# Kernel tuning notes

Measured on AMD Instinct MI355X. Metric: run time of the kernel, lower is better.

## Reference

```python
import jax, jax.numpy as jnp
import numpy as np

EPS = 1e-8
KERNEL_K = 25
SCALES = (1, 2, 3)


def setup_inputs() -> dict:
    key = jax.random.key(0)
    k1, k2, k3 = jax.random.split(key, 3)
    B, D = 4096, 256
    features = jax.random.normal(k1, (B, D), dtype=jnp.float32)
    scores = jax.random.normal(k2, (B, 1), dtype=jnp.float32)
    labels = jax.random.randint(k3, (B,), 0, 6, dtype=jnp.int64)
    return {"features": features, "scores": scores, "labels": labels}


def _affinity(features):
    # squared pairwise euclidean distances (cdist(...,p=2)**2)
    sq = jnp.sum(features * features, axis=1)
    dist_sq = jnp.maximum(sq[:, None] + sq[None, :] - 2.0 * (features @ features.T), 0.0)
    B = features.shape[0]
    k = min(KERNEL_K, B)
    neg_topk, topk_idx = jax.lax.top_k(-dist_sq, k)  # smallest-k per row
    topk_dist = -neg_topk
    sigma = jnp.mean(jnp.sqrt(topk_dist + EPS), axis=1, keepdims=True)  # [B,1]
    sigma_mat = sigma @ sigma.T
    knn_mask = jnp.zeros((B, B), dtype=bool).at[jnp.arange(B)[:, None], topk_idx].set(True)
    mutual = knn_mask & knn_mask.T
    W = jnp.exp(-dist_sq / (sigma_mat + EPS))
    return W * mutual.astype(W.dtype)


def reference(features, scores, labels):
    B = features.shape[0]
    W_feat = _affinity(features)
    lab = labels.reshape(-1, 1).astype(features.dtype)
    direction_mask = (lab <= lab.T).astype(features.dtype)
    W = W_feat * direction_mask + jnp.eye(B, dtype=features.dtype)
    P = W / (jnp.sum(W, axis=1, keepdims=True) + EPS)
    penalty = jax.nn.relu(scores - scores.T)  # [B,B]
    loss = jnp.asarray(0.0, dtype=features.dtype)
    P_t = P
    max_scale = max(SCALES)
    for t in range(1, max_scale + 1):
        if t in SCALES:
            loss = loss + (1.0 / t) * jnp.mean(jnp.sum(P_t * penalty, axis=1))
        if t < max_scale:
            P_t = P_t @ P
    return loss
```

## Files before the change

kernel.cpp:

```cpp
#include <hip/hip_runtime.h>
#include <math.h>
#include <float.h>

#define NB 4096
#define ND 256
#define NK 25
#define EPSF 1e-8f
#define CAP 256

typedef __attribute__((ext_vector_type(8))) short bf16x8;
typedef __attribute__((ext_vector_type(4))) float f32x4;

#define GLD_LDS16(gp, lp)                                                   \
    __builtin_amdgcn_global_load_lds(                                       \
        (const __attribute__((address_space(1))) void*)(uintptr_t)(gp),     \
        (__attribute__((address_space(3))) void*)(uint32_t)(uintptr_t)(lp), \
        16, 0, 0)

__device__ inline short f2bf(float x) {
    unsigned u = __float_as_uint(x);
    return (short)((u + 0x7FFF + ((u >> 16) & 1)) >> 16);
}

__global__ __launch_bounds__(64) void prep_kernel(const float* __restrict__ f,
                                                  short* __restrict__ fh,
                                                  float* __restrict__ sq) {
    int row  = blockIdx.x;
    int lane = threadIdx.x;
    float4 v = ((const float4*)(f + (size_t)row * ND))[lane];
    float acc = v.x * v.x + v.y * v.y + v.z * v.z + v.w * v.w;
    *(short4*)(fh + (size_t)row * ND + lane * 4) =
        make_short4(f2bf(v.x), f2bf(v.y), f2bf(v.z), f2bf(v.w));
#pragma unroll
    for (int off = 32; off; off >>= 1) acc += __shfl_down(acc, off);
    if (lane == 0) sq[row] = acc;
}

#define BM 128
#define BK 64
__global__ __launch_bounds__(256) void gram_kernel(const short* __restrict__ fh,
                                                   const float* __restrict__ sq,
                                                   float* __restrict__ dist) {
    __shared__ __align__(16) short As[BM * BK];
    __shared__ __align__(16) short Bs[BM * BK];
    int b   = blockIdx.x;
    int ti  = (b >> 5) * BM;
    int tj  = (b & 31) * BM;
    int tid = threadIdx.x;
    int w = tid >> 6, lane = tid & 63;
    int wr = w >> 1, wc = w & 1;
    int fr = lane & 15, fq = lane >> 4;

    f32x4 acc[4][4];
#pragma unroll
    for (int m = 0; m < 4; ++m)
#pragma unroll
        for (int n = 0; n < 4; ++n) acc[m][n] = (f32x4){0.f, 0.f, 0.f, 0.f};

    int srow = lane >> 3;
    int scol = (lane & 7) * 8;

    for (int s = 0; s < 4; ++s) {
        int k0 = s * 64;
#pragma unroll
        for (int i = 0; i < 4; ++i) {
            int c   = 4 * w + i;
            int row = c * 8 + srow;
            GLD_LDS16(fh + (size_t)(ti + row) * ND + k0 + scol, As + c * 512);
            GLD_LDS16(fh + (size_t)(tj + row) * ND + k0 + scol, Bs + c * 512);
        }
        __syncthreads();
#pragma unroll
        for (int kk = 0; kk < 2; ++kk) {
            bf16x8 af[4], bfr[4];
#pragma unroll
            for (int m = 0; m < 4; ++m)
                af[m] = *(const bf16x8*)(As + (wr * 64 + m * 16 + fr) * 64 + kk * 32 + fq * 8);
#pragma unroll
            for (int n = 0; n < 4; ++n)
                bfr[n] = *(const bf16x8*)(Bs + (wc * 64 + n * 16 + fr) * 64 + kk * 32 + fq * 8);
#pragma unroll
            for (int m = 0; m < 4; ++m)
#pragma unroll
                for (int n = 0; n < 4; ++n)
                    acc[m][n] = __builtin_amdgcn_mfma_f32_16x16x32_bf16(af[m], bfr[n], acc[m][n], 0, 0, 0);
        }
        __syncthreads();
    }

#pragma unroll
    for (int m = 0; m < 4; ++m) {
#pragma unroll
        for (int j = 0; j < 4; ++j) {
            int gi = ti + wr * 64 + m * 16 + fq * 4 + j;
            float si = sq[gi];
            float* drow = dist + (size_t)gi * NB + tj + wc * 64;
#pragma unroll
            for (int n = 0; n < 4; ++n) {
                float d = si + sq[tj + wc * 64 + n * 16 + fr] - 2.f * acc[m][n][j];
                drow[n * 16 + fr] = fmaxf(d, 0.f);
            }
        }
    }
}

__global__ __launch_bounds__(256) void topk4_kernel(const float* __restrict__ dist,
                                                    int* __restrict__ idxk,
                                                    float* __restrict__ dk,
                                                    float* __restrict__ sigma) {
    int wid  = threadIdx.x >> 6;
    int lane = threadIdx.x & 63;
    int row  = blockIdx.x * 4 + wid;
    __shared__ float cval[4][CAP];
    __shared__ int   cidx[4][CAP];

    float v[64];
    const float4* src = (const float4*)(dist + (size_t)row * NB);
#pragma unroll
    for (int c = 0; c < 16; ++c) {
        float4 q = src[c * 64 + lane];
        v[c * 4 + 0] = q.x; v[c * 4 + 1] = q.y;
        v[c * 4 + 2] = q.z; v[c * 4 + 3] = q.w;
    }

    float mx = v[0], sm = v[0];
#pragma unroll
    for (int e = 1; e < 64; ++e) { mx = fmaxf(mx, v[e]); sm += v[e]; }
#pragma unroll
    for (int off = 32; off; off >>= 1) {
        mx = fmaxf(mx, __shfl_xor(mx, off));
        sm += __shfl_xor(sm, off);
    }
    float mu = sm * (1.0f / NB);

    int c0 = 0;
#pragma unroll
    for (int e = 0; e < 64; ++e) c0 += (v[e] < mu) ? 1 : 0;
#pragma unroll
    for (int off = 32; off; off >>= 1) c0 += __shfl_xor(c0, off);
    float lo = 0.f, hi = mu;
    int cnt_hi = c0;
    if (cnt_hi < NK) { hi = mx * 1.000001f + 1e-20f; cnt_hi = NB; }

    for (int it = 0; it < 40; ++it) {
        if (cnt_hi <= 64) break;
        float mid = 0.5f * (lo + hi);
        if (mid <= lo || mid >= hi) break;
        int c = 0;
#pragma unroll
        for (int e = 0; e < 64; ++e) c += (v[e] < mid) ? 1 : 0;
#pragma unroll
        for (int off = 32; off; off >>= 1) c += __shfl_xor(c, off);
        if (c >= NK) { hi = mid; cnt_hi = c; } else { lo = mid; }
    }

    float Thi = hi;
    unsigned long long ltmask = (1ull << lane) - 1ull;
    int cnt = 0;
#pragma unroll
    for (int e = 0; e < 64; ++e) {
        bool p = (v[e] < Thi);
        unsigned long long m = __ballot(p);
        if (p) {
            int pos = cnt + __popcll(m & ltmask);
            if (pos < CAP) {
                cval[wid][pos] = v[e];
                cidx[wid][pos] = ((e >> 2) * 64 + lane) * 4 + (e & 3);
            }
        }
        cnt += __popcll(m);
    }
    cnt = min(cnt, CAP);

    if (cnt <= 64) {
        float x  = (lane < cnt) ? cval[wid][lane] : FLT_MAX;
        int   xi = (lane < cnt) ? cidx[wid][lane] : 0x7fffffff;
        int rank = 0;
        for (int s = 1; s < 64; ++s) {
            int   sl = (lane + s) & 63;
            float y  = __shfl(x, sl);
            int   yi = __shfl(xi, sl);
            rank += (y < x || (y == x && yi < xi)) ? 1 : 0;
        }
        bool sel = (lane < cnt) && (rank < NK);
        if (sel) {
            idxk[row * NK + rank] = xi;
            dk[row * NK + rank]   = x;
        }
        float t = sel ? sqrtf(x + EPSF) : 0.f;
#pragma unroll
        for (int off = 32; off; off >>= 1) t += __shfl_xor(t, off);
        if (lane == 0) sigma[row] = t * (1.0f / NK);
    } else {
        float ssum = 0.f;
        for (int it = 0; it < NK; ++it) {
            float bv = FLT_MAX; int bi = NB; int bp = -1;
            for (int r = lane; r < cnt; r += 64) {
                float cv = cval[wid][r]; int ci = cidx[wid][r];
                if (cv < bv || (cv == bv && ci < bi)) { bv = cv; bi = ci; bp = r; }
            }
#pragma unroll
            for (int off = 32; off; off >>= 1) {
                float ov = __shfl_xor(bv, off);
                int   oi = __shfl_xor(bi, off);
                int   op = __shfl_xor(bp, off);
                if (ov < bv || (ov == bv && oi < bi)) { bv = ov; bi = oi; bp = op; }
            }
            if (lane == 0) {
                idxk[row * NK + it] = bi;
                dk[row * NK + it]   = bv;
                cval[wid][bp] = FLT_MAX;
            }
            bv = __shfl(bv, 0);
            ssum += sqrtf(bv + EPSF);
        }
        if (lane == 0) sigma[row] = ssum * (1.0f / NK);
    }
}

__global__ __launch_bounds__(64) void buildp_kernel(const int* __restrict__ idxk,
                                                    const float* __restrict__ dk,
                                                    const float* __restrict__ sigma,
                                                    const int* __restrict__ labels,
                                                    const float* __restrict__ scores,
                                                    float* __restrict__ pval,
                                                    float* __restrict__ bs,
                                                    float2* __restrict__ cs) {
    int row  = blockIdx.x;
    int lane = threadIdx.x;
    __shared__ float sb[32];
    __shared__ float sp[32];

    float w = 0.f;
    int j = 0;
    if (lane < NK) {
        j = idxk[row * NK + lane];
        bool mut = false;
        for (int n = 0; n < NK; ++n) mut |= (idxk[j * NK + n] == row);
        bool dir = labels[row] <= labels[j];
        float sij = sigma[row] * sigma[j] + EPSF;
        w = (mut && dir) ? expf(-dk[row * NK + lane] / sij) : 0.f;
        if (j == row) w += 1.f;
    }
    float rs = w;
#pragma unroll
    for (int off = 32; off; off >>= 1) rs += __shfl_down(rs, off);
    rs = __shfl(rs, 0);
    float pv = (lane < NK) ? w / (rs + EPSF) : 0.f;
    if (lane < NK) pval[row * NK + lane] = pv;

    float sj = (lane < NK) ? scores[j] : FLT_MAX;
    int rank = 0;
#pragma unroll
    for (int u = 0; u < NK; ++u) {
        float su = __shfl(sj, u);
        rank += (su < sj || (su == sj && u < lane)) ? 1 : 0;
    }
    if (lane < 32) { sb[lane] = FLT_MAX; sp[lane] = 0.f; }
    __syncthreads();
    if (lane < NK) { sb[rank] = sj; sp[rank] = pv; }
    __syncthreads();

    float b = sb[lane & 31];
    float p = sp[lane & 31];
    float c  = p;
    float s2 = p * b;
#pragma unroll
    for (int off = 1; off < 32; off <<= 1) {
        float oc = __shfl_up(c, off);
        float os = __shfl_up(s2, off);
        if (lane >= off) { c += oc; s2 += os; }
    }
    float ce = __shfl_up(c, 1);
    float se = __shfl_up(s2, 1);
    if (lane == 0) { ce = 0.f; se = 0.f; }
    if (lane < 32) {
        bs[row * 32 + lane] = b;
        cs[row * 32 + lane] = make_float2(ce, se);
    }
}

__global__ __launch_bounds__(256) void hval_kernel(const int* __restrict__ idxk,
                                                   const float* __restrict__ pval,
                                                   const float* __restrict__ scores,
                                                   const float* __restrict__ bs,
                                                   const float2* __restrict__ cs,
                                                   float* __restrict__ Gval,
                                                   float* __restrict__ Hval) {
    int wid  = threadIdx.x >> 6;
    int lane = threadIdx.x & 63;
    int j    = blockIdx.x * 4 + wid;
    __shared__ float2 slab[4][NK][26];

    int  ln = (lane < NK) ? lane : NK - 1;
    int  q  = idxk[j * NK + ln];
    float p = (lane < NK) ? pval[j * NK + lane] : 0.f;
    float sqv = scores[q];

    float4 bq[7];
    const float4* b4 = (const float4*)(bs + q * 32);
#pragma unroll
    for (int t = 0; t < 7; ++t) bq[t] = b4[t];
    const float4* c4 = (const float4*)(cs + q * 32);
    if (lane < NK) {
#pragma unroll
        for (int t = 0; t < 13; ++t)
            *(float4*)&slab[wid][lane][t * 2] = c4[t];
    }

    float bjj = bs[j * 32 + lane];
    int posj = 0;
#pragma unroll
    for (int r = 0; r < NK; ++r)
        posj += (__shfl(bjj, r) < sqv) ? 1 : 0;
    float2 cj = cs[j * 32 + posj];
    if (lane < NK) Gval[j * 32 + lane] = sqv * cj.x - cj.y;

    __syncthreads();

    for (int u = 0; u < NK; ++u) {
        float x = __shfl(sqv, u);
        int pos = 0;
#pragma unroll
        for (int t = 0; t < 7; ++t) {
            float4 b = bq[t];
            pos += (b.x < x) + (b.y < x) + (b.z < x) + (b.w < x);
        }
        float2 ch = slab[wid][ln][pos];
        float g = p * (x * ch.x - ch.y);
#pragma unroll
        for (int off = 32; off; off >>= 1) g += __shfl_xor(g, off);
        if (lane == 0) Hval[j * 32 + u] = g;
    }
}

__global__ __launch_bounds__(256) void loss_kernel(const float* __restrict__ scores,
                                                   const int* __restrict__ idxk,
                                                   const float* __restrict__ pval,
                                                   const float* __restrict__ Gval,
                                                   const float* __restrict__ Hval,
                                                   float* __restrict__ partial) {
    int wid  = threadIdx.x >> 6;
    int lane = threadIdx.x & 63;
    int i    = blockIdx.x * 4 + wid;
    float si = scores[i];
    float acc = 0.f;
    if (lane < NK) {
        int   jm = idxk[i * NK + lane];
        float pm = pval[i * NK + lane];
        float sj = scores[jm];
        int slot = -1;
        const int* row = idxk + jm * NK;
#pragma unroll
        for (int n = 0; n < NK; ++n)
            if (row[n] == i) slot = n;
        float g = 0.f, h = 0.f;
        if (slot >= 0) {
            g = Gval[jm * 32 + slot];
            h = Hval[jm * 32 + slot];
        }
        acc = pm * (fmaxf(si - sj, 0.f) + 0.5f * g + (1.f / 3.f) * h);
    }
#pragma unroll
    for (int off = 32; off; off >>= 1) acc += __shfl_xor(acc, off);
    if (lane == 0) partial[i] = acc;
}

__global__ __launch_bounds__(256) void reduce_kernel(const float* __restrict__ partial,
                                                     float* __restrict__ out) {
    int tid = threadIdx.x;
    __shared__ float red[4];
    float a = 0.f;
    for (int t = tid; t < NB / 4; t += 256) {
        float4 p = ((const float4*)partial)[t];
        a += p.x + p.y + p.z + p.w;
    }
#pragma unroll
    for (int off = 32; off; off >>= 1) a += __shfl_xor(a, off);
    if ((tid & 63) == 0) red[tid >> 6] = a;
    __syncthreads();
    if (tid == 0) out[0] = (red[0] + red[1] + red[2] + red[3]) * (1.0f / NB);
}

extern "C" void kernel_launch(void* const* d_in, const int* in_sizes, int n_in,
                              void* d_out, int out_size, void* d_ws, size_t ws_size,
                              hipStream_t stream) {
    const float* features = (const float*)d_in[0];
    const float* scores   = (const float*)d_in[1];
    const int*   labels   = (const int*)d_in[2];
    float* out = (float*)d_out;

    char* ws = (char*)d_ws;
    size_t off = 0;
    float*  dist    = (float*) (ws + off); off += (size_t)NB * NB * 4;
    short*  fh      = (short*) (ws + off); off += (size_t)NB * ND * 2;
    float*  sq      = (float*) (ws + off); off += (size_t)NB * 4;
    int*    idxk    = (int*)   (ws + off); off += (size_t)NB * NK * 4;
    float*  dk      = (float*) (ws + off); off += (size_t)NB * NK * 4;
    float*  sigma   = (float*) (ws + off); off += (size_t)NB * 4;
    float*  pval    = (float*) (ws + off); off += (size_t)NB * NK * 4;
    float*  bs      = (float*) (ws + off); off += (size_t)NB * 32 * 4;
    float2* cs      = (float2*)(ws + off); off += (size_t)NB * 32 * 8;
    float*  Gval    = (float*) (ws + off); off += (size_t)NB * 32 * 4;
    float*  Hval    = (float*) (ws + off); off += (size_t)NB * 32 * 4;
    float*  partial = (float*) (ws + off); off += (size_t)NB * 4;

    prep_kernel<<<NB, 64, 0, stream>>>(features, fh, sq);
    gram_kernel<<<(NB / BM) * (NB / BM), 256, 0, stream>>>(fh, sq, dist);
    topk4_kernel<<<NB / 4, 256, 0, stream>>>(dist, idxk, dk, sigma);
    buildp_kernel<<<NB, 64, 0, stream>>>(idxk, dk, sigma, labels, scores, pval, bs, cs);
    hval_kernel<<<NB / 4, 256, 0, stream>>>(idxk, pval, scores, bs, cs, Gval, Hval);
    loss_kernel<<<NB / 4, 256, 0, stream>>>(scores, idxk, pval, Gval, Hval, partial);
    reduce_kernel<<<1, 256, 0, stream>>>(partial, out);
}
```

Baseline: 101.4 us.

## Filter kNN candidates in gram epilogue instead of materializing full distance matrix

The gram kernel no longer writes the full 4096x4096 distance matrix. It keeps only entries below a per-row threshold, estimated from the statistics of the squared norms, and appends them to a per-row candidate list with atomics. A small top-k kernel ranks these candidates. Rows whose candidate count falls outside the valid range go to a fallback kernel that recomputes the row in full. This removes a 64MB write and re-read, but adds global atomics, an extra launch of 4096 mostly-idle blocks, and a slow path whose cost depends on how well the threshold fits the data.

```diff
diff --git a/kernel.cpp b/kernel.cpp
--- a/kernel.cpp
+++ b/kernel.cpp
@@ -7,6 +7,8 @@
 #define NK 25
 #define EPSF 1e-8f
 #define CAP 256
+#define CAP_FB 1024
+#define CTGT 192
 
 typedef __attribute__((ext_vector_type(8))) short bf16x8;
 typedef __attribute__((ext_vector_type(4))) float f32x4;
@@ -20,6 +22,9 @@
 __device__ inline short f2bf(float x) {
     unsigned u = __float_as_uint(x);
     return (short)((u + 0x7FFF + ((u >> 16) & 1)) >> 16);
+}
+__device__ inline float bf2f(short s) {
+    return __uint_as_float(((unsigned)(unsigned short)s) << 16);
 }
 
 __global__ __launch_bounds__(64) void prep_kernel(const float* __restrict__ f,
@@ -36,13 +41,40 @@
     if (lane == 0) sq[row] = acc;
 }
 
+__global__ __launch_bounds__(256) void mstat_kernel(const float* __restrict__ sq,
+                                                    float* __restrict__ T,
+                                                    int* __restrict__ cnt,
+                                                    int* __restrict__ flag) {
+    int tid = threadIdx.x;
+    __shared__ float r1[4], r2[4];
+    float a1 = 0.f, a2 = 0.f;
+    for (int t = tid; t < NB; t += 256) { float s = sq[t]; a1 += s; a2 += s * s; }
+#pragma unroll
+    for (int off = 32; off; off >>= 1) { a1 += __shfl_xor(a1, off); a2 += __shfl_xor(a2, off); }
+    if ((tid & 63) == 0) { r1[tid >> 6] = a1; r2[tid >> 6] = a2; }
+    __syncthreads();
+    float M1 = (r1[0] + r1[1] + r1[2] + r1[3]) * (1.0f / NB);
+    float M2 = (r2[0] + r2[1] + r2[2] + r2[3]) * (1.0f / NB);
+    float varsq = fmaxf(M2 - M1 * M1, 0.f);
+    for (int t = tid; t < NB; t += 256) {
+        float s = sq[t];
+        float sig = sqrtf(varsq + 4.f * s);
+        T[t] = s + M1 - 2.0f * sig;
+        cnt[t]  = 0;
+        flag[t] = 0;
+    }
+}
+
 #define BM 128
 #define BK 64
 __global__ __launch_bounds__(256) void gram_kernel(const short* __restrict__ fh,
                                                    const float* __restrict__ sq,
-                                                   float* __restrict__ dist) {
+                                                   const float* __restrict__ T,
+                                                   int* __restrict__ cnt,
+                                                   float2* __restrict__ cand) {
     __shared__ __align__(16) short As[BM * BK];
     __shared__ __align__(16) short Bs[BM * BK];
+    __shared__ float sT[BM];
     int b   = blockIdx.x;
     int ti  = (b >> 5) * BM;
     int tj  = (b & 31) * BM;
@@ -51,6 +83,8 @@
     int wr = w >> 1, wc = w & 1;
     int fr = lane & 15, fq = lane >> 4;
 
+    if (tid < BM) sT[tid] = T[ti + tid];
+
     f32x4 acc[4][4];
 #pragma unroll
     for (int m = 0; m < 4; ++m)
@@ -92,129 +126,170 @@
     for (int m = 0; m < 4; ++m) {
 #pragma unroll
         for (int j = 0; j < 4; ++j) {
-            int gi = ti + wr * 64 + m * 16 + fq * 4 + j;
+            int rl = wr * 64 + m * 16 + fq * 4 + j;
+            int gi = ti + rl;
             float si = sq[gi];
-            float* drow = dist + (size_t)gi * NB + tj + wc * 64;
+            float Tr = sT[rl];
 #pragma unroll
             for (int n = 0; n < 4; ++n) {
-                float d = si + sq[tj + wc * 64 + n * 16 + fr] - 2.f * acc[m][n][j];
-                drow[n * 16 + fr] = fmaxf(d, 0.f);
+                int col = tj + wc * 64 + n * 16 + fr;
+                float d = fmaxf(si + sq[col] - 2.f * acc[m][n][j], 0.f);
+                if (d < Tr) {
+                    int pos = atomicAdd(&cnt[gi], 1);
+                    if (pos < CAP)
+                        cand[(size_t)gi * CAP + pos] = make_float2(d, __int_as_float(col));
+                }
             }
         }
     }
 }
 
-__global__ __launch_bounds__(256) void topk4_kernel(const float* __restrict__ dist,
+__global__ __launch_bounds__(256) void topk5_kernel(const float2* __restrict__ cand,
+                                                    const int* __restrict__ cnt,
+                                                    int* __restrict__ flag,
                                                     int* __restrict__ idxk,
                                                     float* __restrict__ dk,
                                                     float* __restrict__ sigma) {
     int wid  = threadIdx.x >> 6;
     int lane = threadIdx.x & 63;
     int row  = blockIdx.x * 4 + wid;
-    __shared__ float cval[4][CAP];
-    __shared__ int   cidx[4][CAP];
-
-    float v[64];
-    const float4* src = (const float4*)(dist + (size_t)row * NB);
-#pragma unroll
-    for (int c = 0; c < 16; ++c) {
-        float4 q = src[c * 64 + lane];
-        v[c * 4 + 0] = q.x; v[c * 4 + 1] = q.y;
-        v[c * 4 + 2] = q.z; v[c * 4 + 3] = q.w;
-    }
-
-    float mx = v[0], sm = v[0];
-#pragma unroll
-    for (int e = 1; e < 64; ++e) { mx = fmaxf(mx, v[e]); sm += v[e]; }
-#pragma unroll
-    for (int off = 32; off; off >>= 1) {
-        mx = fmaxf(mx, __shfl_xor(mx, off));
-        sm += __shfl_xor(sm, off);
-    }
-    float mu = sm * (1.0f / NB);
-
-    int c0 = 0;
-#pragma unroll
-    for (int e = 0; e < 64; ++e) c0 += (v[e] < mu) ? 1 : 0;
-#pragma unroll
-    for (int off = 32; off; off >>= 1) c0 += __shfl_xor(c0, off);
-    float lo = 0.f, hi = mu;
-    int cnt_hi = c0;
-    if (cnt_hi < NK) { hi = mx * 1.000001f + 1e-20f; cnt_hi = NB; }
-
-    for (int it = 0; it < 40; ++it) {
-        if (cnt_hi <= 64) break;
-        float mid = 0.5f * (lo + hi);
-        if (mid <= lo || mid >= hi) break;
+    int c = cnt[row];
+    if (c < NK || c > CAP) { if (lane == 0) flag[row] = 1; return; }
+    int slots = (c + 63) >> 6;
+
+    float v[4]; int id[4];
+#pragma unroll
+    for (int k = 0; k < 4; ++k) {
+        int p = lane + 64 * k;
+        if (p < c) {
+            float2 q = cand[(size_t)row * CAP + p];
+            v[k] = q.x; id[k] = __float_as_int(q.y);
+        } else { v[k] = FLT_MAX; id[k] = 0x7fffffff; }
+    }
+    int rank[4] = {0, 0, 0, 0};
+    for (int s = 0; s < 64; ++s) {
+        int sl = (lane + s) & 63;
+#pragma unroll
+        for (int k2 = 0; k2 < 4; ++k2) {
+            if (k2 < slots) {
+                float y  = __shfl(v[k2], sl);
+                int   yi = __shfl(id[k2], sl);
+#pragma unroll
+                for (int k = 0; k < 4; ++k) {
+                    if (k < slots) {
+                        bool lt = (y < v[k]) || (y == v[k] && yi < id[k]);
+                        rank[k] += lt ? 1 : 0;
+                    }
+                }
+            }
+        }
+    }
+    float t = 0.f;
+#pragma unroll
+    for (int k = 0; k < 4; ++k) {
+        if (k < slots && v[k] != FLT_MAX && rank[k] < NK) {
+            idxk[row * NK + rank[k]] = id[k];
+            dk[row * NK + rank[k]]   = v[k];
+            t += sqrtf(v[k] + EPSF);
+        }
+    }
+#pragma unroll
+    for (int off = 32; off; off >>= 1) t += __shfl_xor(t, off);
+    if (lane == 0) sigma[row] = t * (1.0f / NK);
+}
+
+__global__ __launch_bounds__(256) void fixup_kernel(const short* __restrict__ fh,
+                                                    const float* __restrict__ sq,
+                                                    const int* __restrict__ flag,
+                                                    int* __restrict__ idxk,
+                                                    float* __restrict__ dk,
+                                                    float* __restrict__ sigma) {
+    int row = blockIdx.x;
+    if (flag[row] == 0) return;
+    __shared__ float rowv[NB];
+    __shared__ float frv[ND];
+    __shared__ float cval[CAP_FB];
+    __shared__ int   cidx[CAP_FB];
+    __shared__ int   red[4];
+    __shared__ float redf[4];
+    __shared__ int   s_cnt;
+    int tid = threadIdx.x;
+
+    for (int a = tid; a < ND; a += 256) frv[a] = bf2f(fh[(size_t)row * ND + a]);
+    __syncthreads();
+    float sqr = sq[row];
+    for (int c = tid; c < NB; c += 256) {
+        const short4* fc4 = (const short4*)(fh + (size_t)c * ND);
+        float acc = 0.f;
+        for (int a4 = 0; a4 < ND / 4; ++a4) {
+            short4 q = fc4[a4];
+            acc += frv[a4 * 4 + 0] * bf2f(q.x) + frv[a4 * 4 + 1] * bf2f(q.y)
+                 + frv[a4 * 4 + 2] * bf2f(q.z) + frv[a4 * 4 + 3] * bf2f(q.w);
+        }
+        rowv[c] = fmaxf(sqr + sq[c] - 2.f * acc, 0.f);
+    }
+    __syncthreads();
+
+    float mx = 0.f;
+    for (int t = tid; t < NB; t += 256) mx = fmaxf(mx, rowv[t]);
+#pragma unroll
+    for (int off = 32; off; off >>= 1) mx = fmaxf(mx, __shfl_xor(mx, off));
+    if ((tid & 63) == 0) redf[tid >> 6] = mx;
+    __syncthreads();
+    mx = fmaxf(fmaxf(redf[0], redf[1]), fmaxf(redf[2], redf[3]));
+
+    unsigned lo = 0u, hi = __float_as_uint(mx) + 1u;
+    int cnt_hi = NB;
+    for (int it = 0; it < 34; ++it) {
+        if (cnt_hi <= CTGT || hi <= lo + 1u) break;
+        unsigned mid = (lo + hi) >> 1;
+        float Tm = __uint_as_float(mid);
         int c = 0;
-#pragma unroll
-        for (int e = 0; e < 64; ++e) c += (v[e] < mid) ? 1 : 0;
+        for (int t = tid; t < NB; t += 256) c += (rowv[t] < Tm) ? 1 : 0;
 #pragma unroll
         for (int off = 32; off; off >>= 1) c += __shfl_xor(c, off);
+        __syncthreads();
+        if ((tid & 63) == 0) red[tid >> 6] = c;
+        __syncthreads();
+        c = red[0] + red[1] + red[2] + red[3];
         if (c >= NK) { hi = mid; cnt_hi = c; } else { lo = mid; }
     }
-
-    float Thi = hi;
-    unsigned long long ltmask = (1ull << lane) - 1ull;
-    int cnt = 0;
-#pragma unroll
-    for (int e = 0; e < 64; ++e) {
-        bool p = (v[e] < Thi);
-        unsigned long long m = __ballot(p);
-        if (p) {
-            int pos = cnt + __popcll(m & ltmask);
-            if (pos < CAP) {
-                cval[wid][pos] = v[e];
-                cidx[wid][pos] = ((e >> 2) * 64 + lane) * 4 + (e & 3);
-            }
-        }
-        cnt += __popcll(m);
-    }
-    cnt = min(cnt, CAP);
-
-    if (cnt <= 64) {
-        float x  = (lane < cnt) ? cval[wid][lane] : FLT_MAX;
-        int   xi = (lane < cnt) ? cidx[wid][lane] : 0x7fffffff;
-        int rank = 0;
-        for (int s = 1; s < 64; ++s) {
-            int   sl = (lane + s) & 63;
-            float y  = __shfl(x, sl);
-            int   yi = __shfl(xi, sl);
-            rank += (y < x || (y == x && yi < xi)) ? 1 : 0;
-        }
-        bool sel = (lane < cnt) && (rank < NK);
-        if (sel) {
-            idxk[row * NK + rank] = xi;
-            dk[row * NK + rank]   = x;
-        }
-        float t = sel ? sqrtf(x + EPSF) : 0.f;
-#pragma unroll
-        for (int off = 32; off; off >>= 1) t += __shfl_xor(t, off);
-        if (lane == 0) sigma[row] = t * (1.0f / NK);
-    } else {
+    float Thi = __uint_as_float(hi);
+    if (tid == 0) s_cnt = 0;
+    __syncthreads();
+    for (int t = tid; t < NB; t += 256) {
+        if (rowv[t] < Thi) {
+            int p = atomicAdd(&s_cnt, 1);
+            if (p < CAP_FB) { cval[p] = rowv[t]; cidx[p] = t; }
+        }
+    }
+    __syncthreads();
+    int cnt = min(s_cnt, CAP_FB);
+
+    if (tid < 64) {
         float ssum = 0.f;
         for (int it = 0; it < NK; ++it) {
             float bv = FLT_MAX; int bi = NB; int bp = -1;
-            for (int r = lane; r < cnt; r += 64) {
-                float cv = cval[wid][r]; int ci = cidx[wid][r];
+            for (int r = tid; r < cnt; r += 64) {
+                float cv = cval[r]; int ci = cidx[r];
                 if (cv < bv || (cv == bv && ci < bi)) { bv = cv; bi = ci; bp = r; }
             }
 #pragma unroll
             for (int off = 32; off; off >>= 1) {
-                float ov = __shfl_xor(bv, off);
-                int   oi = __shfl_xor(bi, off);
-                int   op = __shfl_xor(bp, off);
+                float ov = __shfl_down(bv, off);
+                int   oi = __shfl_down(bi, off);
+                int   op = __shfl_down(bp, off);
                 if (ov < bv || (ov == bv && oi < bi)) { bv = ov; bi = oi; bp = op; }
             }
-            if (lane == 0) {
+            bp = __shfl(bp, 0); bv = __shfl(bv, 0); bi = __shfl(bi, 0);
+            if (tid == 0) {
                 idxk[row * NK + it] = bi;
                 dk[row * NK + it]   = bv;
-                cval[wid][bp] = FLT_MAX;
+                cval[bp] = FLT_MAX;
             }
-            bv = __shfl(bv, 0);
             ssum += sqrtf(bv + EPSF);
         }
-        if (lane == 0) sigma[row] = ssum * (1.0f / NK);
+        if (tid == 0) sigma[row] = ssum * (1.0f / NK);
     }
 }
 
@@ -392,9 +467,12 @@
 
     char* ws = (char*)d_ws;
     size_t off = 0;
-    float*  dist    = (float*) (ws + off); off += (size_t)NB * NB * 4;
+    float2* cand    = (float2*)(ws + off); off += (size_t)NB * CAP * 8;
     short*  fh      = (short*) (ws + off); off += (size_t)NB * ND * 2;
     float*  sq      = (float*) (ws + off); off += (size_t)NB * 4;
+    float*  T       = (float*) (ws + off); off += (size_t)NB * 4;
+    int*    cnt     = (int*)   (ws + off); off += (size_t)NB * 4;
+    int*    flag    = (int*)   (ws + off); off += (size_t)NB * 4;
     int*    idxk    = (int*)   (ws + off); off += (size_t)NB * NK * 4;
     float*  dk      = (float*) (ws + off); off += (size_t)NB * NK * 4;
     float*  sigma   = (float*) (ws + off); off += (size_t)NB * 4;
@@ -406,8 +484,10 @@
     float*  partial = (float*) (ws + off); off += (size_t)NB * 4;
 
     prep_kernel<<<NB, 64, 0, stream>>>(features, fh, sq);
-    gram_kernel<<<(NB / BM) * (NB / BM), 256, 0, stream>>>(fh, sq, dist);
-    topk4_kernel<<<NB / 4, 256, 0, stream>>>(dist, idxk, dk, sigma);
+    mstat_kernel<<<1, 256, 0, stream>>>(sq, T, cnt, flag);
+    gram_kernel<<<(NB / BM) * (NB / BM), 256, 0, stream>>>(fh, sq, T, cnt, cand);
+    topk5_kernel<<<NB / 4, 256, 0, stream>>>(cand, cnt, flag, idxk, dk, sigma);
+    fixup_kernel<<<NB, 256, 0, stream>>>(fh, sq, flag, idxk, dk, sigma);
     buildp_kernel<<<NB, 64, 0, stream>>>(idxk, dk, sigma, labels, scores, pval, bs, cs);
     hval_kernel<<<NB / 4, 256, 0, stream>>>(idxk, pval, scores, bs, cs, Gval, Hval);
     loss_kernel<<<NB / 4, 256, 0, stream>>>(scores, idxk, pval, Gval, Hval, partial);
```

Measured after the change: 173.4 us. 70.9% more time.

## Predict per-row top-k threshold from norm statistics and use block-per-row selection

Applied to the files above, without the earlier changes.

Adds a small kernel that estimates, for each row, a distance threshold from the mean and variance of squared norms. The top-k kernel then filters candidates against that threshold in a single pass, falling back to bisection only when the candidate count falls outside [NK, CAP]. The kernel moves from one wavefront per row to one 256-thread block per row, which gathers candidates with shared-memory atomics and ranks them by counting. This removes the usual bisection passes over the row but depends on the threshold holding for Gaussian-like inputs; the fallback keeps the result exact.

```diff
diff --git a/kernel.cpp b/kernel.cpp
--- a/kernel.cpp
+++ b/kernel.cpp
@@ -34,6 +34,25 @@
 #pragma unroll
     for (int off = 32; off; off >>= 1) acc += __shfl_down(acc, off);
     if (lane == 0) sq[row] = acc;
+}
+
+__global__ __launch_bounds__(256) void mstat_kernel(const float* __restrict__ sq,
+                                                    float* __restrict__ T) {
+    int tid = threadIdx.x;
+    __shared__ float r1[4], r2[4];
+    float a1 = 0.f, a2 = 0.f;
+    for (int t = tid; t < NB; t += 256) { float s = sq[t]; a1 += s; a2 += s * s; }
+#pragma unroll
+    for (int off = 32; off; off >>= 1) { a1 += __shfl_xor(a1, off); a2 += __shfl_xor(a2, off); }
+    if ((tid & 63) == 0) { r1[tid >> 6] = a1; r2[tid >> 6] = a2; }
+    __syncthreads();
+    float M1 = (r1[0] + r1[1] + r1[2] + r1[3]) * (1.0f / NB);
+    float M2 = (r2[0] + r2[1] + r2[2] + r2[3]) * (1.0f / NB);
+    float varsq = fmaxf(M2 - M1 * M1, 0.f);
+    for (int t = tid; t < NB; t += 256) {
+        float s = sq[t];
+        T[t] = s + M1 - 2.0f * sqrtf(varsq + 4.f * s);
+    }
 }
 
 #define BM 128
@@ -104,117 +123,116 @@
     }
 }
 
-__global__ __launch_bounds__(256) void topk4_kernel(const float* __restrict__ dist,
+__global__ __launch_bounds__(256) void topk8_kernel(const float* __restrict__ dist,
+                                                    const float* __restrict__ T,
                                                     int* __restrict__ idxk,
                                                     float* __restrict__ dk,
                                                     float* __restrict__ sigma) {
-    int wid  = threadIdx.x >> 6;
-    int lane = threadIdx.x & 63;
-    int row  = blockIdx.x * 4 + wid;
-    __shared__ float cval[4][CAP];
-    __shared__ int   cidx[4][CAP];
-
-    float v[64];
+    int row = blockIdx.x;
+    int tid = threadIdx.x;
+    __shared__ float cval[CAP];
+    __shared__ int   cidx[CAP];
+    __shared__ float ssq[NK];
+    __shared__ int   s_cnt;
+    __shared__ int   red[4];
+
+    if (tid == 0) s_cnt = 0;
+    __syncthreads();
+
+    float Tr = T[row];
     const float4* src = (const float4*)(dist + (size_t)row * NB);
-#pragma unroll
-    for (int c = 0; c < 16; ++c) {
-        float4 q = src[c * 64 + lane];
-        v[c * 4 + 0] = q.x; v[c * 4 + 1] = q.y;
-        v[c * 4 + 2] = q.z; v[c * 4 + 3] = q.w;
-    }
-
-    float mx = v[0], sm = v[0];
-#pragma unroll
-    for (int e = 1; e < 64; ++e) { mx = fmaxf(mx, v[e]); sm += v[e]; }
-#pragma unroll
-    for (int off = 32; off; off >>= 1) {
-        mx = fmaxf(mx, __shfl_xor(mx, off));
-        sm += __shfl_xor(sm, off);
-    }
-    float mu = sm * (1.0f / NB);
-
-    int c0 = 0;
-#pragma unroll
-    for (int e = 0; e < 64; ++e) c0 += (v[e] < mu) ? 1 : 0;
-#pragma unroll
-    for (int off = 32; off; off >>= 1) c0 += __shfl_xor(c0, off);
-    float lo = 0.f, hi = mu;
-    int cnt_hi = c0;
-    if (cnt_hi < NK) { hi = mx * 1.000001f + 1e-20f; cnt_hi = NB; }
-
-    for (int it = 0; it < 40; ++it) {
-        if (cnt_hi <= 64) break;
-        float mid = 0.5f * (lo + hi);
-        if (mid <= lo || mid >= hi) break;
-        int c = 0;
-#pragma unroll
-        for (int e = 0; e < 64; ++e) c += (v[e] < mid) ? 1 : 0;
-#pragma unroll
-        for (int off = 32; off; off >>= 1) c += __shfl_xor(c, off);
-        if (c >= NK) { hi = mid; cnt_hi = c; } else { lo = mid; }
-    }
-
-    float Thi = hi;
-    unsigned long long ltmask = (1ull << lane) - 1ull;
-    int cnt = 0;
-#pragma unroll
-    for (int e = 0; e < 64; ++e) {
-        bool p = (v[e] < Thi);
-        unsigned long long m = __ballot(p);
-        if (p) {
-            int pos = cnt + __popcll(m & ltmask);
+
+    float4 q0 = src[0 * 256 + tid];
+    float4 q1 = src[1 * 256 + tid];
+    float4 q2 = src[2 * 256 + tid];
+    float4 q3 = src[3 * 256 + tid];
+    float xs[16] = {q0.x, q0.y, q0.z, q0.w, q1.x, q1.y, q1.z, q1.w,
+                    q2.x, q2.y, q2.z, q2.w, q3.x, q3.y, q3.z, q3.w};
+#pragma unroll
+    for (int e = 0; e < 16; ++e) {
+        if (xs[e] < Tr) {
+            int pos = atomicAdd(&s_cnt, 1);
             if (pos < CAP) {
-                cval[wid][pos] = v[e];
-                cidx[wid][pos] = ((e >> 2) * 64 + lane) * 4 + (e & 3);
+                cval[pos] = xs[e];
+                cidx[pos] = ((e >> 2) * 256 + tid) * 4 + (e & 3);
             }
         }
-        cnt += __popcll(m);
-    }
-    cnt = min(cnt, CAP);
-
-    if (cnt <= 64) {
-        float x  = (lane < cnt) ? cval[wid][lane] : FLT_MAX;
-        int   xi = (lane < cnt) ? cidx[wid][lane] : 0x7fffffff;
-        int rank = 0;
-        for (int s = 1; s < 64; ++s) {
-            int   sl = (lane + s) & 63;
-            float y  = __shfl(x, sl);
-            int   yi = __shfl(xi, sl);
-            rank += (y < x || (y == x && yi < xi)) ? 1 : 0;
-        }
-        bool sel = (lane < cnt) && (rank < NK);
-        if (sel) {
-            idxk[row * NK + rank] = xi;
-            dk[row * NK + rank]   = x;
-        }
-        float t = sel ? sqrtf(x + EPSF) : 0.f;
-#pragma unroll
-        for (int off = 32; off; off >>= 1) t += __shfl_xor(t, off);
-        if (lane == 0) sigma[row] = t * (1.0f / NK);
-    } else {
-        float ssum = 0.f;
-        for (int it = 0; it < NK; ++it) {
-            float bv = FLT_MAX; int bi = NB; int bp = -1;
-            for (int r = lane; r < cnt; r += 64) {
-                float cv = cval[wid][r]; int ci = cidx[wid][r];
-                if (cv < bv || (cv == bv && ci < bi)) { bv = cv; bi = ci; bp = r; }
+    }
+    __syncthreads();
+    int cnt = s_cnt;
+
+    if (cnt < NK || cnt > CAP) {
+        float s1 = 0.f, mx = 0.f;
+#pragma unroll
+        for (int e = 0; e < 16; ++e) { s1 += xs[e]; mx = fmaxf(mx, xs[e]); }
+#pragma unroll
+        for (int off = 32; off; off >>= 1) { s1 += __shfl_xor(s1, off); mx = fmaxf(mx, __shfl_xor(mx, off)); }
+        __syncthreads();
+        if ((tid & 63) == 0) { ((float*)red)[tid >> 6] = s1; }
+        __syncthreads();
+        s1 = ((float*)red)[0] + ((float*)red)[1] + ((float*)red)[2] + ((float*)red)[3];
+        __syncthreads();
+        if ((tid & 63) == 0) { ((float*)red)[tid >> 6] = mx; }
+        __syncthreads();
+        mx = fmaxf(fmaxf(((float*)red)[0], ((float*)red)[1]),
+                   fmaxf(((float*)red)[2], ((float*)red)[3]));
+        float mu = s1 * (1.0f / NB);
+        float lo = 0.f, hi = mx * 1.000001f + 1e-20f;
+        int cnt_hi = NB;
+        for (int it = 0; it < 40; ++it) {
+            if (cnt_hi >= NK && cnt_hi <= CAP) break;
+            float mid = (cnt_hi > CAP) ? 0.5f * (lo + hi) : mu;
+            mid = 0.5f * (lo + hi);
+            if (mid <= lo || mid >= hi) break;
+            int c = 0;
+#pragma unroll
+            for (int e = 0; e < 16; ++e) c += (xs[e] < mid) ? 1 : 0;
+#pragma unroll
+            for (int off = 32; off; off >>= 1) c += __shfl_xor(c, off);
+            __syncthreads();
+            if ((tid & 63) == 0) red[tid >> 6] = c;
+            __syncthreads();
+            c = red[0] + red[1] + red[2] + red[3];
+            if (c >= NK) { hi = mid; cnt_hi = c; } else { lo = mid; }
+            __syncthreads();
+        }
+        Tr = hi;
+        if (tid == 0) s_cnt = 0;
+        __syncthreads();
+#pragma unroll
+        for (int e = 0; e < 16; ++e) {
+            if (xs[e] < Tr) {
+                int pos = atomicAdd(&s_cnt, 1);
+                if (pos < CAP) {
+                    cval[pos] = xs[e];
+                    cidx[pos] = ((e >> 2) * 256 + tid) * 4 + (e & 3);
+                }
             }
-#pragma unroll
-            for (int off = 32; off; off >>= 1) {
-                float ov = __shfl_xor(bv, off);
-                int   oi = __shfl_xor(bi, off);
-                int   op = __shfl_xor(bp, off);
-                if (ov < bv || (ov == bv && oi < bi)) { bv = ov; bi = oi; bp = op; }
-            }
-            if (lane == 0) {
-                idxk[row * NK + it] = bi;
-                dk[row * NK + it]   = bv;
-                cval[wid][bp] = FLT_MAX;
-            }
-            bv = __shfl(bv, 0);
-            ssum += sqrtf(bv + EPSF);
-        }
-        if (lane == 0) sigma[row] = ssum * (1.0f / NK);
+        }
+        __syncthreads();
+        cnt = min(s_cnt, CAP);
+    }
+
+    float x  = (tid < cnt) ? cval[tid] : FLT_MAX;
+    int   xi = (tid < cnt) ? cidx[tid] : 0x7fffffff;
+    int rank = 0;
+    for (int r = 0; r < cnt; ++r) {
+        float y  = cval[r];
+        int   yi = cidx[r];
+        rank += (y < x || (y == x && yi < xi)) ? 1 : 0;
+    }
+    bool sel = (tid < cnt) && (rank < NK);
+    if (sel) {
+        idxk[row * NK + rank] = xi;
+        dk[row * NK + rank]   = x;
+        ssq[rank] = sqrtf(x + EPSF);
+    }
+    __syncthreads();
+    if (tid == 0) {
+        float t = 0.f;
+#pragma unroll
+        for (int r = 0; r < NK; ++r) t += ssq[r];
+        sigma[row] = t * (1.0f / NK);
     }
 }
 
@@ -395,6 +413,7 @@
     float*  dist    = (float*) (ws + off); off += (size_t)NB * NB * 4;
     short*  fh      = (short*) (ws + off); off += (size_t)NB * ND * 2;
     float*  sq      = (float*) (ws + off); off += (size_t)NB * 4;
+    float*  T       = (float*) (ws + off); off += (size_t)NB * 4;
     int*    idxk    = (int*)   (ws + off); off += (size_t)NB * NK * 4;
     float*  dk      = (float*) (ws + off); off += (size_t)NB * NK * 4;
     float*  sigma   = (float*) (ws + off); off += (size_t)NB * 4;
@@ -406,8 +425,9 @@
     float*  partial = (float*) (ws + off); off += (size_t)NB * 4;
 
     prep_kernel<<<NB, 64, 0, stream>>>(features, fh, sq);
+    mstat_kernel<<<1, 256, 0, stream>>>(sq, T);
     gram_kernel<<<(NB / BM) * (NB / BM), 256, 0, stream>>>(fh, sq, dist);
-    topk4_kernel<<<NB / 4, 256, 0, stream>>>(dist, idxk, dk, sigma);
+    topk8_kernel<<<NB, 256, 0, stream>>>(dist, T, idxk, dk, sigma);
     buildp_kernel<<<NB, 64, 0, stream>>>(idxk, dk, sigma, labels, scores, pval, bs, cs);
     hval_kernel<<<NB / 4, 256, 0, stream>>>(idxk, pval, scores, bs, cs, Gval, Hval);
     loss_kernel<<<NB / 4, 256, 0, stream>>>(scores, idxk, pval, Gval, Hval, partial);
```

Result: slower. 113.2 us (+11.6%).
